# Kernel tuning notes

Measured on AMD Instinct MI355X. Metric: run time of the kernel, lower is better.

The kernel has to match this reference:

```python
import jax, jax.numpy as jnp
import numpy as np

N, E, F_IN, HID, HEADS, OUT = 50000, 800000, 128, 128, 2, 1
NEG_SLOPE = 0.2


def setup_inputs() -> dict:
    key = jax.random.key(0)
    ks = jax.random.split(key, 10)
    x = jax.random.normal(ks[0], (N, F_IN), jnp.float32)
    x = x.at[0, 0].set(0.0)  # ensure a root node (x[:,0]==0)
    edge_index = jax.random.randint(ks[1], (2, E), 0, N, dtype=jnp.int64)
    s = 0.05
    return {
        "x": x,
        "edge_index": edge_index,
        "Wl": jax.random.normal(ks[2], (4, F_IN, HEADS * HID), jnp.float32) * s,
        "bl": jnp.zeros((4, HEADS * HID), jnp.float32),
        "Wr": jax.random.normal(ks[3], (4, F_IN, HEADS * HID), jnp.float32) * s,
        "br": jnp.zeros((4, HEADS * HID), jnp.float32),
        "att": jax.random.normal(ks[4], (4, HEADS, HID), jnp.float32) * s,
        "bias": jnp.zeros((4, HID), jnp.float32),
        "fcW": jax.random.normal(ks[5], (HID, OUT), jnp.float32) * s,
        "fcb": jnp.zeros((OUT,), jnp.float32),
    }


def _gatv2(x, src, dst, Wl, bl, Wr, br, att, bias):
    n = x.shape[0]
    H, C = att.shape
    xl = (x @ Wl + bl).reshape(n, H, C)   # source transform
    xr = (x @ Wr + br).reshape(n, H, C)   # target transform
    # per-edge attention logits: a^T LeakyReLU(xl[j] + xr[i])
    e = jnp.einsum('ehc,hc->eh', jax.nn.leaky_relu(xl[src] + xr[dst], NEG_SLOPE), att)
    # segment softmax over incoming edges of each target node
    m = jax.ops.segment_max(e, dst, num_segments=n)
    m = jnp.where(jnp.isfinite(m), m, 0.0)
    p = jnp.exp(e - m[dst])
    denom = jax.ops.segment_sum(p, dst, num_segments=n)
    alpha = p / (denom[dst] + 1e-16)      # [E, H]
    msg = alpha[:, :, None] * xl[src]      # [E, H, C]
    out = jax.ops.segment_sum(msg.reshape(-1, H * C), dst, num_segments=n).reshape(n, H, C)
    return out.mean(axis=1) + bias         # concat=False -> head mean + bias


def reference(x, edge_index, Wl, bl, Wr, br, att, bias, fcW, fcb):
    src, dst = edge_index[0], edge_index[1]
    h = x
    for l in range(4):
        h = _gatv2(h, src, dst, Wl[l], bl[l], Wr[l], br[l], att[l], bias[l])
        h = jax.nn.relu(h)  # dropout is identity in eval mode
    out = jax.nn.sigmoid(h @ fcW + fcb)    # mode='root_probability', use_log_prob=False
    root_idx = jnp.argmax(x[:, 0] == 0.0)  # first root node
    return out[root_idx][None, :]          # [1, out_channels]
```

## Files before the change

kernel.cpp:

```cpp
#include <hip/hip_runtime.h>


__global__ __launch_bounds__(256) void init_k(int N, int* __restrict__ level,
                                              int* __restrict__ cnt,
                                              int* __restrict__ srcflag,
                                              int* __restrict__ nctr,
                                              int* __restrict__ list0) {
    int gtid = blockIdx.x * blockDim.x + threadIdx.x;
    int gs = gridDim.x * blockDim.x;
    for (int i = gtid; i < N; i += gs) {
        level[i] = 0x7fffffff; cnt[i] = 0; srcflag[i] = 0;
    }
    if (gtid == 0) {
        level[0] = 0;
        list0[0] = 0;
        for (int j = 0; j < 8; ++j) nctr[j] = 0;
        nctr[0] = 1;
    }
}

__global__ __launch_bounds__(256) void bfs_k(const int* __restrict__ ei, int E, int N,
                                             int* __restrict__ level, int k) {
    int e = blockIdx.x * blockDim.x + threadIdx.x;
    if (e < E) {
        int d = ei[E + e];
        int s = ei[e];
        if ((unsigned)d < (unsigned)N && (unsigned)s < (unsigned)N) {
            if (level[d] <= k - 1 && level[s] > k) level[s] = k;
        }
    }
}

__global__ __launch_bounds__(256) void flag_count_k(const int* __restrict__ ei, int E, int N,
                                                    const int* __restrict__ level,
                                                    int* __restrict__ cnt,
                                                    int* __restrict__ srcflag) {
    int e = blockIdx.x * blockDim.x + threadIdx.x;
    if (e < E) {
        int d = ei[E + e];
        int s = ei[e];
        if ((unsigned)d < (unsigned)N && (unsigned)s < (unsigned)N && level[d] <= 3) {
            atomicAdd(&cnt[d], 1);
            srcflag[s] = 1;
        }
    }
}

__global__ __launch_bounds__(256) void block_sum_k(const int* __restrict__ cnt, int n,
                                                   int* __restrict__ bsum) {
    __shared__ int s[256];
    int base = blockIdx.x * 1024;
    int sum = 0;
    for (int i = threadIdx.x; i < 1024; i += 256) {
        int j = base + i;
        sum += (j < n) ? cnt[j] : 0;
    }
    s[threadIdx.x] = sum;
    __syncthreads();
    for (int off = 128; off > 0; off >>= 1) {
        if (threadIdx.x < (unsigned)off) s[threadIdx.x] += s[threadIdx.x + off];
        __syncthreads();
    }
    if (threadIdx.x == 0) bsum[blockIdx.x] = s[0];
}

__global__ __launch_bounds__(64) void scan_bsum_k(int* __restrict__ bsum, int nb,
                                                  int* __restrict__ rowptr, int n) {
    if (threadIdx.x == 0) {
        int acc = 0;
        for (int i = 0; i < nb; ++i) { int v = bsum[i]; bsum[i] = acc; acc += v; }
        rowptr[n] = acc;
    }
}

__global__ __launch_bounds__(1024) void scan_final_k(const int* __restrict__ cnt, int n,
                                                     const int* __restrict__ bsum,
                                                     int* __restrict__ rowptr) {
    __shared__ int s[1024];
    int i = blockIdx.x * 1024 + threadIdx.x;
    int v = (i < n) ? cnt[i] : 0;
    s[threadIdx.x] = v;
    __syncthreads();
    for (int off = 1; off < 1024; off <<= 1) {
        int t = (threadIdx.x >= (unsigned)off) ? s[threadIdx.x - off] : 0;
        __syncthreads();
        s[threadIdx.x] += t;
        __syncthreads();
    }
    if (i < n) rowptr[i] = bsum[blockIdx.x] + s[threadIdx.x] - v;
}

__global__ __launch_bounds__(256) void fill_csr_k(const int* __restrict__ ei, int E, int N,
                                                  const int* __restrict__ level,
                                                  const int* __restrict__ rowptr,
                                                  int* __restrict__ cnt,
                                                  int* __restrict__ csr_src) {
    int e = blockIdx.x * blockDim.x + threadIdx.x;
    if (e < E) {
        int d = ei[E + e];
        int s = ei[e];
        if ((unsigned)d < (unsigned)N && (unsigned)s < (unsigned)N && level[d] <= 3) {
            int pos = rowptr[d] + atomicSub(&cnt[d], 1) - 1;
            csr_src[pos] = s;
        }
    }
}

__global__ __launch_bounds__(256) void build_lists_k(const int* __restrict__ level,
                                                     const int* __restrict__ srcflag, int N,
                                                     int* __restrict__ l1,
                                                     int* __restrict__ l2,
                                                     int* __restrict__ l3,
                                                     int* __restrict__ l4,
                                                     int* __restrict__ nctr) {
    int i = blockIdx.x * blockDim.x + threadIdx.x;
    if (i < N) {
        int l = level[i];
        if (l <= 3) {
            l3[atomicAdd(&nctr[3], 1)] = i;
            if (l <= 2) {
                l2[atomicAdd(&nctr[2], 1)] = i;
                if (l <= 1) l1[atomicAdd(&nctr[1], 1)] = i;
            }
        }
        if (srcflag[i]) l4[atomicAdd(&nctr[4], 1)] = i;
    }
}

__device__ __forceinline__ void gemm_body(const float* __restrict__ A,
                                          const float* __restrict__ W,
                                          const float* __restrict__ b,
                                          float* __restrict__ out,
                                          const int* __restrict__ list,
                                          const int* __restrict__ pcnt,
                                          int bid, int RG,
                                          float (*Wl)[64], int* rows_s) {
    int count = *pcnt;
    int cgi = bid & 3, rg = bid >> 2;
    int tid = threadIdx.x;
    int c0 = cgi * 64;
    for (int i = tid; i < 2048; i += 256) {
        int kk = i >> 4, j = (i & 15) * 4;
        *(float4*)&Wl[kk][j] = *(const float4*)&W[(size_t)kk * 256 + c0 + j];
    }
    int csl = (tid & 7) * 8;
    int rsl = (tid >> 3) * 4;
    float4 bv0 = *(const float4*)&b[c0 + csl];
    float4 bv1 = *(const float4*)&b[c0 + csl + 4];
    for (int base = rg * 128; base < count; base += RG * 128) {
        __syncthreads();
        if (tid < 128) rows_s[tid] = (base + tid < count) ? list[base + tid] : -1;
        __syncthreads();
        int gr[4];
#pragma unroll
        for (int r = 0; r < 4; ++r) gr[r] = rows_s[rsl + r];
        float acc[4][8];
#pragma unroll
        for (int r = 0; r < 4; ++r)
#pragma unroll
            for (int cc = 0; cc < 8; ++cc) acc[r][cc] = 0.f;
        for (int k = 0; k < 128; k += 4) {
            float4 a4[4];
#pragma unroll
            for (int r = 0; r < 4; ++r) {
                int g = gr[r] < 0 ? 0 : gr[r];
                a4[r] = *(const float4*)&A[(size_t)g * 128 + k];
            }
#pragma unroll
            for (int j = 0; j < 4; ++j) {
                float4 w0 = *(const float4*)&Wl[k + j][csl];
                float4 w1 = *(const float4*)&Wl[k + j][csl + 4];
#pragma unroll
                for (int r = 0; r < 4; ++r) {
                    float a = ((const float*)&a4[r])[j];
                    acc[r][0] += a * w0.x; acc[r][1] += a * w0.y;
                    acc[r][2] += a * w0.z; acc[r][3] += a * w0.w;
                    acc[r][4] += a * w1.x; acc[r][5] += a * w1.y;
                    acc[r][6] += a * w1.z; acc[r][7] += a * w1.w;
                }
            }
        }
#pragma unroll
        for (int r = 0; r < 4; ++r) {
            int g = gr[r];
            if (g >= 0) {
                float4 o0, o1;
                o0.x = acc[r][0] + bv0.x; o0.y = acc[r][1] + bv0.y;
                o0.z = acc[r][2] + bv0.z; o0.w = acc[r][3] + bv0.w;
                o1.x = acc[r][4] + bv1.x; o1.y = acc[r][5] + bv1.y;
                o1.z = acc[r][6] + bv1.z; o1.w = acc[r][7] + bv1.w;
                *(float4*)&out[(size_t)g * 256 + c0 + csl]     = o0;
                *(float4*)&out[(size_t)g * 256 + c0 + csl + 4] = o1;
            }
        }
    }
}

__global__ __launch_bounds__(256) void gemm_pair_k(
    const float* __restrict__ A,
    const float* __restrict__ Wa, const float* __restrict__ ba,
    float* __restrict__ oa, const int* __restrict__ la,
    const int* __restrict__ ca, int RGa,
    const float* __restrict__ Wb, const float* __restrict__ bb,
    float* __restrict__ ob, const int* __restrict__ lb,
    const int* __restrict__ cb, int RGb) {
    __shared__ float Wl[128][64];
    __shared__ int rows_s[128];
    int bid = blockIdx.x;
    if (bid < 4 * RGa) gemm_body(A, Wa, ba, oa, la, ca, bid, RGa, Wl, rows_s);
    else gemm_body(A, Wb, bb, ob, lb, cb, bid - 4 * RGa, RGb, Wl, rows_s);
}

__global__ __launch_bounds__(256) void aggregate_list_k(
    const float* __restrict__ xl, const float* __restrict__ xr,
    const int* __restrict__ rowptr, const int* __restrict__ csr,
    const float* __restrict__ att, const float* __restrict__ bias,
    float* __restrict__ hout, const int* __restrict__ list,
    const int* __restrict__ pcnt) {
    int count = *pcnt;
    int wid = (int)((blockIdx.x * blockDim.x + threadIdx.x) >> 6);
    int nw  = (int)((gridDim.x * blockDim.x) >> 6);
    int lane = threadIdx.x & 63;
    const float4* xl4 = (const float4*)xl;
    float4 atv = ((const float4*)att)[lane];
    for (int w = wid; w < count; w += nw) {
        int node = list[w];
        float4 xrv = ((const float4*)xr)[(size_t)node * 64 + lane];
        float m = -3.4e38f, denom = 0.f;
        float ax = 0.f, ay = 0.f, az = 0.f, aw = 0.f;
        int beg = rowptr[node], end = rowptr[node + 1];
        for (int e = beg; e < end; ++e) {
            int src = csr[e];
            float4 a = xl4[(size_t)src * 64 + lane];
            float vx = a.x + xrv.x; vx = vx > 0.f ? vx : 0.2f * vx;
            float vy = a.y + xrv.y; vy = vy > 0.f ? vy : 0.2f * vy;
            float vz = a.z + xrv.z; vz = vz > 0.f ? vz : 0.2f * vz;
            float vw = a.w + xrv.w; vw = vw > 0.f ? vw : 0.2f * vw;
            float p = vx * atv.x + vy * atv.y + vz * atv.z + vw * atv.w;
            p += __shfl_xor(p, 1);
            p += __shfl_xor(p, 2);
            p += __shfl_xor(p, 4);
            p += __shfl_xor(p, 8);
            p += __shfl_xor(p, 16);
            float mn = fmaxf(m, p);
            float scale = __expf(m - mn);
            float wgt = __expf(p - mn);
            m = mn;
            denom = denom * scale + wgt;
            ax = ax * scale + wgt * a.x;
            ay = ay * scale + wgt * a.y;
            az = az * scale + wgt * a.z;
            aw = aw * scale + wgt * a.w;
        }
        float inv = 1.0f / (denom + 1e-16f);
        float ox = ax * inv, oy = ay * inv, oz = az * inv, ow = aw * inv;
        float px = __shfl_xor(ox, 32);
        float py = __shfl_xor(oy, 32);
        float pz = __shfl_xor(oz, 32);
        float pw = __shfl_xor(ow, 32);
        if (lane < 32) {
            float4 bv = ((const float4*)bias)[lane];
            float4 r;
            r.x = fmaxf(0.5f * (ox + px) + bv.x, 0.f);
            r.y = fmaxf(0.5f * (oy + py) + bv.y, 0.f);
            r.z = fmaxf(0.5f * (oz + pz) + bv.z, 0.f);
            r.w = fmaxf(0.5f * (ow + pw) + bv.w, 0.f);
            ((float4*)hout)[(size_t)node * 32 + lane] = r;
        }
    }
}

__global__ __launch_bounds__(64) void agg_final_k(
    const float* __restrict__ xl, const float* __restrict__ xr,
    const int* __restrict__ rowptr, const int* __restrict__ csr,
    const float* __restrict__ att, const float* __restrict__ bias,
    const float* __restrict__ fcW, const float* __restrict__ fcb,
    float* __restrict__ out) {
    int lane = threadIdx.x & 63;
    const float4* xl4 = (const float4*)xl;
    float4 atv = ((const float4*)att)[lane];
    float4 xrv = ((const float4*)xr)[lane];
    float m = -3.4e38f, denom = 0.f;
    float ax = 0.f, ay = 0.f, az = 0.f, aw = 0.f;
    int beg = rowptr[0], end = rowptr[1];
    for (int e = beg; e < end; ++e) {
        int src = csr[e];
        float4 a = xl4[(size_t)src * 64 + lane];
        float vx = a.x + xrv.x; vx = vx > 0.f ? vx : 0.2f * vx;
        float vy = a.y + xrv.y; vy = vy > 0.f ? vy : 0.2f * vy;
        float vz = a.z + xrv.z; vz = vz > 0.f ? vz : 0.2f * vz;
        float vw = a.w + xrv.w; vw = vw > 0.f ? vw : 0.2f * vw;
        float p = vx * atv.x + vy * atv.y + vz * atv.z + vw * atv.w;
        p += __shfl_xor(p, 1);
        p += __shfl_xor(p, 2);
        p += __shfl_xor(p, 4);
        p += __shfl_xor(p, 8);
        p += __shfl_xor(p, 16);
        float mn = fmaxf(m, p);
        float scale = __expf(m - mn);
        float wgt = __expf(p - mn);
        m = mn;
        denom = denom * scale + wgt;
        ax = ax * scale + wgt * a.x;
        ay = ay * scale + wgt * a.y;
        az = az * scale + wgt * a.z;
        aw = aw * scale + wgt * a.w;
    }
    float inv = 1.0f / (denom + 1e-16f);
    float ox = ax * inv, oy = ay * inv, oz = az * inv, ow = aw * inv;
    float px = __shfl_xor(ox, 32);
    float py = __shfl_xor(oy, 32);
    float pz = __shfl_xor(oz, 32);
    float pw = __shfl_xor(ow, 32);
    float partial = 0.f;
    if (lane < 32) {
        float4 bv = ((const float4*)bias)[lane];
        float hx = fmaxf(0.5f * (ox + px) + bv.x, 0.f);
        float hy = fmaxf(0.5f * (oy + py) + bv.y, 0.f);
        float hz = fmaxf(0.5f * (oz + pz) + bv.z, 0.f);
        float hw = fmaxf(0.5f * (ow + pw) + bv.w, 0.f);
        partial = hx * fcW[4 * lane] + hy * fcW[4 * lane + 1] +
                  hz * fcW[4 * lane + 2] + hw * fcW[4 * lane + 3];
    }
    partial += __shfl_xor(partial, 1);
    partial += __shfl_xor(partial, 2);
    partial += __shfl_xor(partial, 4);
    partial += __shfl_xor(partial, 8);
    partial += __shfl_xor(partial, 16);
    partial += __shfl_xor(partial, 32);
    if (lane == 0) out[0] = 1.f / (1.f + __expf(-(partial + fcb[0])));
}

extern "C" void kernel_launch(void* const* d_in, const int* in_sizes, int n_in,
                              void* d_out, int out_size, void* d_ws, size_t ws_size,
                              hipStream_t stream) {
    const float* x    = (const float*)d_in[0];
    const int*   ei   = (const int*)d_in[1];
    const float* Wlw  = (const float*)d_in[2];
    const float* blw  = (const float*)d_in[3];
    const float* Wrw  = (const float*)d_in[4];
    const float* brw  = (const float*)d_in[5];
    const float* att  = (const float*)d_in[6];
    const float* bias = (const float*)d_in[7];
    const float* fcW  = (const float*)d_in[8];
    const float* fcb  = (const float*)d_in[9];
    int N = in_sizes[0] / 128;
    int E = in_sizes[1] / 2;
    int nb = (N + 1023) / 1024;

    char* ws = (char*)d_ws;
    size_t off = 0;
    auto alloc = [&](size_t bytes) -> void* {
        void* p = ws + off;
        off += (bytes + 255) & ~(size_t)255;
        return p;
    };
    float* h       = (float*)alloc((size_t)N * 128 * 4);
    float* xl      = (float*)alloc((size_t)N * 256 * 4);
    float* xr      = (float*)alloc((size_t)N * 256 * 4);
    int*   csr     = (int*)alloc((size_t)E * 4);
    int*   rowptr  = (int*)alloc((size_t)(N + 1) * 4);
    int*   cnt     = (int*)alloc((size_t)N * 4);
    int*   srcflag = (int*)alloc((size_t)N * 4);
    int*   nctr    = (int*)alloc(256);
    int*   level   = (int*)alloc((size_t)N * 4);
    int*   list0   = (int*)alloc(64 * 4);
    int*   list1   = (int*)alloc((size_t)N * 4);
    int*   list2   = (int*)alloc((size_t)N * 4);
    int*   list3   = (int*)alloc((size_t)N * 4);
    int*   list4   = (int*)alloc((size_t)N * 4);
    int*   bsum    = (int*)alloc(64 * 4);

    init_k<<<256, 256, 0, stream>>>(N, level, cnt, srcflag, nctr, list0);
    for (int k = 1; k <= 3; ++k)
        bfs_k<<<(E + 255) / 256, 256, 0, stream>>>(ei, E, N, level, k);
    flag_count_k<<<(E + 255) / 256, 256, 0, stream>>>(ei, E, N, level, cnt, srcflag);
    block_sum_k<<<nb, 256, 0, stream>>>(cnt, N, bsum);
    scan_bsum_k<<<1, 64, 0, stream>>>(bsum, nb, rowptr, N);
    scan_final_k<<<nb, 1024, 0, stream>>>(cnt, N, bsum, rowptr);
    fill_csr_k<<<(E + 255) / 256, 256, 0, stream>>>(ei, E, N, level, rowptr, cnt, csr);
    build_lists_k<<<(N + 255) / 256, 256, 0, stream>>>(level, srcflag, N,
                                                       list1, list2, list3, list4, nctr);

    const int RG4 = (50000 + 127) / 128;
    const int RG3 = 40, RG2 = 4, RG1 = 1, RG0 = 1;
    gemm_pair_k<<<4 * (RG4 + RG3), 256, 0, stream>>>(
        x, Wlw, blw, xl, list4, nctr + 4, RG4,
        Wrw, brw, xr, list3, nctr + 3, RG3);
    aggregate_list_k<<<1024, 256, 0, stream>>>(xl, xr, rowptr, csr, att, bias, h,
                                               list3, nctr + 3);
    gemm_pair_k<<<4 * (RG3 + RG2), 256, 0, stream>>>(
        h, Wlw + 1 * 128 * 256, blw + 1 * 256, xl, list3, nctr + 3, RG3,
        Wrw + 1 * 128 * 256, brw + 1 * 256, xr, list2, nctr + 2, RG2);
    aggregate_list_k<<<128, 256, 0, stream>>>(xl, xr, rowptr, csr, att + 256,
                                              bias + 128, h, list2, nctr + 2);
    gemm_pair_k<<<4 * (RG2 + RG1), 256, 0, stream>>>(
        h, Wlw + 2 * 128 * 256, blw + 2 * 256, xl, list2, nctr + 2, RG2,
        Wrw + 2 * 128 * 256, brw + 2 * 256, xr, list1, nctr + 1, RG1);
    aggregate_list_k<<<16, 256, 0, stream>>>(xl, xr, rowptr, csr, att + 2 * 256,
                                             bias + 2 * 128, h, list1, nctr + 1);
    gemm_pair_k<<<4 * (RG1 + RG0), 256, 0, stream>>>(
        h, Wlw + 3 * 128 * 256, blw + 3 * 256, xl, list1, nctr + 1, RG1,
        Wrw + 3 * 128 * 256, brw + 3 * 256, xr, list0, nctr + 0, RG0);
    agg_final_k<<<1, 64, 0, stream>>>(xl, xr, rowptr, csr, att + 3 * 256,
                                      bias + 3 * 128, fcW, fcb, (float*)d_out);
}
```

Baseline: 262.0 us.

## Fuse list building into block sum, drop scan kernel, merge tail layers

Folds the node-list construction into the block-sum kernel. Each scan block now recomputes its own prefix from bsum, which removes the single-thread scan kernel. The last-layer aggregation, the layer-4 GEMM for the root's neighbours and the final aggregation are merged into one single-block tail kernel, cutting several launches. The GEMM is retiled to 32-column by 256-row tiles with an early exit for idle blocks, and grid sizes are adjusted. The risk is that the serial tail kernel does all of its GEMM work in one block.

```diff
diff --git a/kernel.cpp b/kernel.cpp
--- a/kernel.cpp
+++ b/kernel.cpp
@@ -46,14 +46,32 @@
     }
 }
 
-__global__ __launch_bounds__(256) void block_sum_k(const int* __restrict__ cnt, int n,
-                                                   int* __restrict__ bsum) {
+__global__ __launch_bounds__(256) void bsum_lists_k(const int* __restrict__ cnt, int n,
+                                                    int* __restrict__ bsum,
+                                                    const int* __restrict__ level,
+                                                    const int* __restrict__ srcflag,
+                                                    int* __restrict__ l1,
+                                                    int* __restrict__ l2,
+                                                    int* __restrict__ l3,
+                                                    int* __restrict__ l4,
+                                                    int* __restrict__ nctr) {
     __shared__ int s[256];
     int base = blockIdx.x * 1024;
     int sum = 0;
     for (int i = threadIdx.x; i < 1024; i += 256) {
         int j = base + i;
-        sum += (j < n) ? cnt[j] : 0;
+        if (j < n) {
+            sum += cnt[j];
+            int l = level[j];
+            if (l <= 3) {
+                l3[atomicAdd(&nctr[3], 1)] = j;
+                if (l <= 2) {
+                    l2[atomicAdd(&nctr[2], 1)] = j;
+                    if (l <= 1) l1[atomicAdd(&nctr[1], 1)] = j;
+                }
+            }
+            if (srcflag[j]) l4[atomicAdd(&nctr[4], 1)] = j;
+        }
     }
     s[threadIdx.x] = sum;
     __syncthreads();
@@ -64,19 +82,16 @@
     if (threadIdx.x == 0) bsum[blockIdx.x] = s[0];
 }
 
-__global__ __launch_bounds__(64) void scan_bsum_k(int* __restrict__ bsum, int nb,
-                                                  int* __restrict__ rowptr, int n) {
-    if (threadIdx.x == 0) {
-        int acc = 0;
-        for (int i = 0; i < nb; ++i) { int v = bsum[i]; bsum[i] = acc; acc += v; }
-        rowptr[n] = acc;
-    }
-}
-
 __global__ __launch_bounds__(1024) void scan_final_k(const int* __restrict__ cnt, int n,
-                                                     const int* __restrict__ bsum,
+                                                     const int* __restrict__ bsum, int nb,
                                                      int* __restrict__ rowptr) {
     __shared__ int s[1024];
+    __shared__ int chunk_base;
+    if (threadIdx.x == 0) {
+        int a = 0;
+        for (int i = 0; i < (int)blockIdx.x; ++i) a += bsum[i];
+        chunk_base = a;
+    }
     int i = blockIdx.x * 1024 + threadIdx.x;
     int v = (i < n) ? cnt[i] : 0;
     s[threadIdx.x] = v;
@@ -87,7 +102,9 @@
         s[threadIdx.x] += t;
         __syncthreads();
     }
-    if (i < n) rowptr[i] = bsum[blockIdx.x] + s[threadIdx.x] - v;
+    if (i < n) rowptr[i] = chunk_base + s[threadIdx.x] - v;
+    if ((int)blockIdx.x == nb - 1 && threadIdx.x == 1023)
+        rowptr[n] = chunk_base + s[1023];
 }
 
 __global__ __launch_bounds__(256) void fill_csr_k(const int* __restrict__ ei, int E, int N,
@@ -106,27 +123,6 @@
     }
 }
 
-__global__ __launch_bounds__(256) void build_lists_k(const int* __restrict__ level,
-                                                     const int* __restrict__ srcflag, int N,
-                                                     int* __restrict__ l1,
-                                                     int* __restrict__ l2,
-                                                     int* __restrict__ l3,
-                                                     int* __restrict__ l4,
-                                                     int* __restrict__ nctr) {
-    int i = blockIdx.x * blockDim.x + threadIdx.x;
-    if (i < N) {
-        int l = level[i];
-        if (l <= 3) {
-            l3[atomicAdd(&nctr[3], 1)] = i;
-            if (l <= 2) {
-                l2[atomicAdd(&nctr[2], 1)] = i;
-                if (l <= 1) l1[atomicAdd(&nctr[1], 1)] = i;
-            }
-        }
-        if (srcflag[i]) l4[atomicAdd(&nctr[4], 1)] = i;
-    }
-}
-
 __device__ __forceinline__ void gemm_body(const float* __restrict__ A,
                                           const float* __restrict__ W,
                                           const float* __restrict__ b,
@@ -134,22 +130,23 @@
                                           const int* __restrict__ list,
                                           const int* __restrict__ pcnt,
                                           int bid, int RG,
-                                          float (*Wl)[64], int* rows_s) {
+                                          float (*Wl)[32], int* rows_s) {
     int count = *pcnt;
-    int cgi = bid & 3, rg = bid >> 2;
+    int cgi = bid & 7, rg = bid >> 3;
+    if (rg * 256 >= count) return;
     int tid = threadIdx.x;
-    int c0 = cgi * 64;
-    for (int i = tid; i < 2048; i += 256) {
-        int kk = i >> 4, j = (i & 15) * 4;
+    int c0 = cgi * 32;
+    for (int i = tid; i < 1024; i += 256) {
+        int kk = i >> 3, j = (i & 7) * 4;
         *(float4*)&Wl[kk][j] = *(const float4*)&W[(size_t)kk * 256 + c0 + j];
     }
-    int csl = (tid & 7) * 8;
-    int rsl = (tid >> 3) * 4;
+    int csl = (tid & 3) * 8;
+    int rsl = (tid >> 2) * 4;
     float4 bv0 = *(const float4*)&b[c0 + csl];
     float4 bv1 = *(const float4*)&b[c0 + csl + 4];
-    for (int base = rg * 128; base < count; base += RG * 128) {
+    for (int base = rg * 256; base < count; base += RG * 256) {
         __syncthreads();
-        if (tid < 128) rows_s[tid] = (base + tid < count) ? list[base + tid] : -1;
+        rows_s[tid] = (base + tid < count) ? list[base + tid] : -1;
         __syncthreads();
         int gr[4];
 #pragma unroll
@@ -204,11 +201,61 @@
     const float* __restrict__ Wb, const float* __restrict__ bb,
     float* __restrict__ ob, const int* __restrict__ lb,
     const int* __restrict__ cb, int RGb) {
-    __shared__ float Wl[128][64];
-    __shared__ int rows_s[128];
+    __shared__ float Wl[128][32];
+    __shared__ int rows_s[256];
     int bid = blockIdx.x;
-    if (bid < 4 * RGa) gemm_body(A, Wa, ba, oa, la, ca, bid, RGa, Wl, rows_s);
-    else gemm_body(A, Wb, bb, ob, lb, cb, bid - 4 * RGa, RGb, Wl, rows_s);
+    if (bid < 8 * RGa) gemm_body(A, Wa, ba, oa, la, ca, bid, RGa, Wl, rows_s);
+    else gemm_body(A, Wb, bb, ob, lb, cb, bid - 8 * RGa, RGb, Wl, rows_s);
+}
+
+__device__ __forceinline__ void agg_node(const float4* __restrict__ xl4,
+                                         const float* __restrict__ xr,
+                                         const int* __restrict__ rowptr,
+                                         const int* __restrict__ csr,
+                                         float4 atv, const float* __restrict__ bias,
+                                         float* __restrict__ hout, int node, int lane) {
+    float4 xrv = ((const float4*)xr)[(size_t)node * 64 + lane];
+    float m = -3.4e38f, denom = 0.f;
+    float ax = 0.f, ay = 0.f, az = 0.f, aw = 0.f;
+    int beg = rowptr[node], end = rowptr[node + 1];
+    for (int e = beg; e < end; ++e) {
+        int src = csr[e];
+        float4 a = xl4[(size_t)src * 64 + lane];
+        float vx = a.x + xrv.x; vx = vx > 0.f ? vx : 0.2f * vx;
+        float vy = a.y + xrv.y; vy = vy > 0.f ? vy : 0.2f * vy;
+        float vz = a.z + xrv.z; vz = vz > 0.f ? vz : 0.2f * vz;
+        float vw = a.w + xrv.w; vw = vw > 0.f ? vw : 0.2f * vw;
+        float p = vx * atv.x + vy * atv.y + vz * atv.z + vw * atv.w;
+        p += __shfl_xor(p, 1);
+        p += __shfl_xor(p, 2);
+        p += __shfl_xor(p, 4);
+        p += __shfl_xor(p, 8);
+        p += __shfl_xor(p, 16);
+        float mn = fmaxf(m, p);
+        float scale = __expf(m - mn);
+        float wgt = __expf(p - mn);
+        m = mn;
+        denom = denom * scale + wgt;
+        ax = ax * scale + wgt * a.x;
+        ay = ay * scale + wgt * a.y;
+        az = az * scale + wgt * a.z;
+        aw = aw * scale + wgt * a.w;
+    }
+    float inv = 1.0f / (denom + 1e-16f);
+    float ox = ax * inv, oy = ay * inv, oz = az * inv, ow = aw * inv;
+    float px = __shfl_xor(ox, 32);
+    float py = __shfl_xor(oy, 32);
+    float pz = __shfl_xor(oz, 32);
+    float pw = __shfl_xor(ow, 32);
+    if (lane < 32) {
+        float4 bv = ((const float4*)bias)[lane];
+        float4 r;
+        r.x = fmaxf(0.5f * (ox + px) + bv.x, 0.f);
+        r.y = fmaxf(0.5f * (oy + py) + bv.y, 0.f);
+        r.z = fmaxf(0.5f * (oz + pz) + bv.z, 0.f);
+        r.w = fmaxf(0.5f * (ow + pw) + bv.w, 0.f);
+        ((float4*)hout)[(size_t)node * 32 + lane] = r;
+    }
 }
 
 __global__ __launch_bounds__(256) void aggregate_list_k(
@@ -223,12 +270,51 @@
     int lane = threadIdx.x & 63;
     const float4* xl4 = (const float4*)xl;
     float4 atv = ((const float4*)att)[lane];
-    for (int w = wid; w < count; w += nw) {
-        int node = list[w];
-        float4 xrv = ((const float4*)xr)[(size_t)node * 64 + lane];
+    for (int w = wid; w < count; w += nw)
+        agg_node(xl4, xr, rowptr, csr, atv, bias, hout, list[w], lane);
+}
+
+__global__ __launch_bounds__(256) void tail_k(
+    float* __restrict__ xl, float* __restrict__ xr,
+    const int* __restrict__ rowptr, const int* __restrict__ csr,
+    const float* __restrict__ att3, const float* __restrict__ bias3,
+    float* __restrict__ h,
+    const float* __restrict__ Wl4, const float* __restrict__ bl4,
+    const float* __restrict__ Wr4, const float* __restrict__ br4,
+    const float* __restrict__ att4, const float* __restrict__ bias4,
+    const float* __restrict__ fcW, const float* __restrict__ fcb,
+    const int* __restrict__ list1, const int* __restrict__ pcnt1,
+    float* __restrict__ out) {
+    int tid = threadIdx.x;
+    int lane = tid & 63;
+    int cnt1 = *pcnt1;
+    const float4* xl4 = (const float4*)xl;
+    {
+        float4 atv = ((const float4*)att3)[lane];
+        for (int w = (tid >> 6); w < cnt1; w += 4)
+            agg_node(xl4, xr, rowptr, csr, atv, bias3, h, list1[w], lane);
+    }
+    __syncthreads();
+    {
+        for (int rw = 0; rw < cnt1; ++rw) {
+            int g = list1[rw];
+            const float* hr = &h[(size_t)g * 128];
+            float acc = 0.f;
+            for (int k = 0; k < 128; ++k) acc += hr[k] * Wl4[(size_t)k * 256 + tid];
+            xl[(size_t)g * 256 + tid] = acc + bl4[tid];
+        }
+        const float* hr = &h[0];
+        float acc = 0.f;
+        for (int k = 0; k < 128; ++k) acc += hr[k] * Wr4[(size_t)k * 256 + tid];
+        xr[tid] = acc + br4[tid];
+    }
+    __syncthreads();
+    if (tid < 64) {
+        float4 atv = ((const float4*)att4)[lane];
+        float4 xrv = ((const float4*)xr)[lane];
         float m = -3.4e38f, denom = 0.f;
         float ax = 0.f, ay = 0.f, az = 0.f, aw = 0.f;
-        int beg = rowptr[node], end = rowptr[node + 1];
+        int beg = rowptr[0], end = rowptr[1];
         for (int e = beg; e < end; ++e) {
             int src = csr[e];
             float4 a = xl4[(size_t)src * 64 + lane];
@@ -258,77 +344,24 @@
         float py = __shfl_xor(oy, 32);
         float pz = __shfl_xor(oz, 32);
         float pw = __shfl_xor(ow, 32);
+        float partial = 0.f;
         if (lane < 32) {
-            float4 bv = ((const float4*)bias)[lane];
-            float4 r;
-            r.x = fmaxf(0.5f * (ox + px) + bv.x, 0.f);
-            r.y = fmaxf(0.5f * (oy + py) + bv.y, 0.f);
-            r.z = fmaxf(0.5f * (oz + pz) + bv.z, 0.f);
-            r.w = fmaxf(0.5f * (ow + pw) + bv.w, 0.f);
-            ((float4*)hout)[(size_t)node * 32 + lane] = r;
-        }
-    }
-}
-
-__global__ __launch_bounds__(64) void agg_final_k(
-    const float* __restrict__ xl, const float* __restrict__ xr,
-    const int* __restrict__ rowptr, const int* __restrict__ csr,
-    const float* __restrict__ att, const float* __restrict__ bias,
-    const float* __restrict__ fcW, const float* __restrict__ fcb,
-    float* __restrict__ out) {
-    int lane = threadIdx.x & 63;
-    const float4* xl4 = (const float4*)xl;
-    float4 atv = ((const float4*)att)[lane];
-    float4 xrv = ((const float4*)xr)[lane];
-    float m = -3.4e38f, denom = 0.f;
-    float ax = 0.f, ay = 0.f, az = 0.f, aw = 0.f;
-    int beg = rowptr[0], end = rowptr[1];
-    for (int e = beg; e < end; ++e) {
-        int src = csr[e];
-        float4 a = xl4[(size_t)src * 64 + lane];
-        float vx = a.x + xrv.x; vx = vx > 0.f ? vx : 0.2f * vx;
-        float vy = a.y + xrv.y; vy = vy > 0.f ? vy : 0.2f * vy;
-        float vz = a.z + xrv.z; vz = vz > 0.f ? vz : 0.2f * vz;
-        float vw = a.w + xrv.w; vw = vw > 0.f ? vw : 0.2f * vw;
-        float p = vx * atv.x + vy * atv.y + vz * atv.z + vw * atv.w;
-        p += __shfl_xor(p, 1);
-        p += __shfl_xor(p, 2);
-        p += __shfl_xor(p, 4);
-        p += __shfl_xor(p, 8);
-        p += __shfl_xor(p, 16);
-        float mn = fmaxf(m, p);
-        float scale = __expf(m - mn);
-        float wgt = __expf(p - mn);
-        m = mn;
-        denom = denom * scale + wgt;
-        ax = ax * scale + wgt * a.x;
-        ay = ay * scale + wgt * a.y;
-        az = az * scale + wgt * a.z;
-        aw = aw * scale + wgt * a.w;
-    }
-    float inv = 1.0f / (denom + 1e-16f);
-    float ox = ax * inv, oy = ay * inv, oz = az * inv, ow = aw * inv;
-    float px = __shfl_xor(ox, 32);
-    float py = __shfl_xor(oy, 32);
-    float pz = __shfl_xor(oz, 32);
-    float pw = __shfl_xor(ow, 32);
-    float partial = 0.f;
-    if (lane < 32) {
-        float4 bv = ((const float4*)bias)[lane];
-        float hx = fmaxf(0.5f * (ox + px) + bv.x, 0.f);
-        float hy = fmaxf(0.5f * (oy + py) + bv.y, 0.f);
-        float hz = fmaxf(0.5f * (oz + pz) + bv.z, 0.f);
-        float hw = fmaxf(0.5f * (ow + pw) + bv.w, 0.f);
-        partial = hx * fcW[4 * lane] + hy * fcW[4 * lane + 1] +
-                  hz * fcW[4 * lane + 2] + hw * fcW[4 * lane + 3];
-    }
-    partial += __shfl_xor(partial, 1);
-    partial += __shfl_xor(partial, 2);
-    partial += __shfl_xor(partial, 4);
-    partial += __shfl_xor(partial, 8);
-    partial += __shfl_xor(partial, 16);
-    partial += __shfl_xor(partial, 32);
-    if (lane == 0) out[0] = 1.f / (1.f + __expf(-(partial + fcb[0])));
+            float4 bv = ((const float4*)bias4)[lane];
+            float hx = fmaxf(0.5f * (ox + px) + bv.x, 0.f);
+            float hy = fmaxf(0.5f * (oy + py) + bv.y, 0.f);
+            float hz = fmaxf(0.5f * (oz + pz) + bv.z, 0.f);
+            float hw = fmaxf(0.5f * (ow + pw) + bv.w, 0.f);
+            partial = hx * fcW[4 * lane] + hy * fcW[4 * lane + 1] +
+                      hz * fcW[4 * lane + 2] + hw * fcW[4 * lane + 3];
+        }
+        partial += __shfl_xor(partial, 1);
+        partial += __shfl_xor(partial, 2);
+        partial += __shfl_xor(partial, 4);
+        partial += __shfl_xor(partial, 8);
+        partial += __shfl_xor(partial, 16);
+        partial += __shfl_xor(partial, 32);
+        if (lane == 0) out[0] = 1.f / (1.f + __expf(-(partial + fcb[0])));
+    }
 }
 
 extern "C" void kernel_launch(void* const* d_in, const int* in_sizes, int n_in,
@@ -371,37 +404,32 @@
     int*   list4   = (int*)alloc((size_t)N * 4);
     int*   bsum    = (int*)alloc(64 * 4);
 
-    init_k<<<256, 256, 0, stream>>>(N, level, cnt, srcflag, nctr, list0);
+    init_k<<<128, 256, 0, stream>>>(N, level, cnt, srcflag, nctr, list0);
     for (int k = 1; k <= 3; ++k)
         bfs_k<<<(E + 255) / 256, 256, 0, stream>>>(ei, E, N, level, k);
     flag_count_k<<<(E + 255) / 256, 256, 0, stream>>>(ei, E, N, level, cnt, srcflag);
-    block_sum_k<<<nb, 256, 0, stream>>>(cnt, N, bsum);
-    scan_bsum_k<<<1, 64, 0, stream>>>(bsum, nb, rowptr, N);
-    scan_final_k<<<nb, 1024, 0, stream>>>(cnt, N, bsum, rowptr);
+    bsum_lists_k<<<nb, 256, 0, stream>>>(cnt, N, bsum, level, srcflag,
+                                         list1, list2, list3, list4, nctr);
+    scan_final_k<<<nb, 1024, 0, stream>>>(cnt, N, bsum, nb, rowptr);
     fill_csr_k<<<(E + 255) / 256, 256, 0, stream>>>(ei, E, N, level, rowptr, cnt, csr);
-    build_lists_k<<<(N + 255) / 256, 256, 0, stream>>>(level, srcflag, N,
-                                                       list1, list2, list3, list4, nctr);
-
-    const int RG4 = (50000 + 127) / 128;
-    const int RG3 = 40, RG2 = 4, RG1 = 1, RG0 = 1;
-    gemm_pair_k<<<4 * (RG4 + RG3), 256, 0, stream>>>(
+
+    const int RG4 = (50000 + 255) / 256;
+    const int RG3 = 18, RG2 = 2, RG1 = 1;
+    gemm_pair_k<<<8 * (RG4 + RG3), 256, 0, stream>>>(
         x, Wlw, blw, xl, list4, nctr + 4, RG4,
         Wrw, brw, xr, list3, nctr + 3, RG3);
     aggregate_list_k<<<1024, 256, 0, stream>>>(xl, xr, rowptr, csr, att, bias, h,
                                                list3, nctr + 3);
-    gemm_pair_k<<<4 * (RG3 + RG2), 256, 0, stream>>>(
+    gemm_pair_k<<<8 * (RG3 + RG2), 256, 0, stream>>>(
         h, Wlw + 1 * 128 * 256, blw + 1 * 256, xl, list3, nctr + 3, RG3,
         Wrw + 1 * 128 * 256, brw + 1 * 256, xr, list2, nctr + 2, RG2);
     aggregate_list_k<<<128, 256, 0, stream>>>(xl, xr, rowptr, csr, att + 256,
                                               bias + 128, h, list2, nctr + 2);
-    gemm_pair_k<<<4 * (RG2 + RG1), 256, 0, stream>>>(
+    gemm_pair_k<<<8 * (RG2 + RG1), 256, 0, stream>>>(
         h, Wlw + 2 * 128 * 256, blw + 2 * 256, xl, list2, nctr + 2, RG2,
         Wrw + 2 * 128 * 256, brw + 2 * 256, xr, list1, nctr + 1, RG1);
-    aggregate_list_k<<<16, 256, 0, stream>>>(xl, xr, rowptr, csr, att + 2 * 256,
-                                             bias + 2 * 128, h, list1, nctr + 1);
-    gemm_pair_k<<<4 * (RG1 + RG0), 256, 0, stream>>>(
-        h, Wlw + 3 * 128 * 256, blw + 3 * 256, xl, list1, nctr + 1, RG1,
-        Wrw + 3 * 128 * 256, brw + 3 * 256, xr, list0, nctr + 0, RG0);
-    agg_final_k<<<1, 64, 0, stream>>>(xl, xr, rowptr, csr, att + 3 * 256,
-                                      bias + 3 * 128, fcW, fcb, (float*)d_out);
-}
+    tail_k<<<1, 256, 0, stream>>>(
+        xl, xr, rowptr, csr, att + 2 * 256, bias + 2 * 128, h,
+        Wlw + 3 * 128 * 256, blw + 3 * 256, Wrw + 3 * 128 * 256, brw + 3 * 256,
+        att + 3 * 256, bias + 3 * 128, fcW, fcb, list1, nctr + 1, (float*)d_out);
+}
```

Measured after the change: 403.2 us. 53.9% more time.
